# Optimization experiments

Hardware: AMD Instinct MI355X
Metric: run time of the kernel (lower is better)

Reference implementation:

```python
import jax, jax.numpy as jnp
import numpy as np

T, B, H = 256, 64, 1024

def setup_inputs() -> dict:
    key = jax.random.key(0)
    k0, k1, k2, k3 = jax.random.split(key, 4)
    x = jax.random.normal(k0, (T, B, H), dtype=jnp.float32)
    # episode resets are sparse events
    resets = jax.random.bernoulli(k1, 0.01, (T, B))
    h0 = jnp.zeros((B, H), dtype=jnp.float32)  # flax GRUCell.initialize_carry -> zeros
    s = np.float32(1.0 / np.sqrt(H))
    Wi = jax.random.normal(k2, (H, 3 * H), dtype=jnp.float32) * s  # packed [ir|iz|in]
    Wh = jax.random.normal(k3, (H, 3 * H), dtype=jnp.float32) * s  # packed [hr|hz|hn]
    bi = jnp.zeros((3 * H,), dtype=jnp.float32)
    bn = jnp.zeros((H,), dtype=jnp.float32)  # only the 'n' hidden dense has a bias in flax
    return dict(x=x, resets=resets, h0=h0, Wi=Wi, bi=bi, Wh=Wh, bn=bn)

def reference(x, resets, h0, Wi, bi, Wh, bn):
    """Scanned GRU with reset masking, matching flax nn.scan(GRUCell)."""
    def step(h, inp):
        x_t, r_t = inp  # [B,H], [B]
        h = jnp.where(r_t[:, None], jnp.zeros_like(h), h)  # reset carry to initial (zeros)
        gi = x_t @ Wi + bi          # [B,3H]
        gh = h @ Wh                 # [B,3H]
        ir, iz, inn = jnp.split(gi, 3, axis=-1)
        hr, hz, hn = jnp.split(gh, 3, axis=-1)
        r = jax.nn.sigmoid(ir + hr)
        z = jax.nn.sigmoid(iz + hz)
        n = jnp.tanh(inn + r * (hn + bn))
        h_new = (1.0 - z) * n + z * h
        return h_new, h_new  # GRUCell returns (new_state, y=new_state)
    h_final, ys = jax.lax.scan(step, h0, (x, resets))
    return h_final, ys
```

## Files before the change

kernel.cpp:

```cpp
#include <hip/hip_runtime.h>
#include <hip/hip_bf16.h>
#include <cstdint>


#define TT 256
#define BB 64
#define HH 1024
#define H3 3072

typedef __attribute__((ext_vector_type(8))) short s16x8;
typedef __attribute__((ext_vector_type(4))) float f32x4;
typedef __attribute__((ext_vector_type(4))) unsigned int u32x4;
typedef unsigned long long ull;

__device__ __forceinline__ float fast_sigmoid(float x) {
  float e = __expf(-fabsf(x));
  float s = 1.0f / (1.0f + e);
  return x >= 0.0f ? s : 1.0f - s;
}
__device__ __forceinline__ float fast_tanh(float x) {
  float e = __expf(-2.0f * fabsf(x));
  float t = (1.0f - e) / (1.0f + e);
  return x >= 0.0f ? t : -t;
}
__device__ __forceinline__ f32x4 mfma16(s16x8 a, s16x8 b, f32x4 c) {
  return __builtin_amdgcn_mfma_f32_16x16x32_bf16(a, b, c, 0, 0, 0);
}

#define LD8(p) __hip_atomic_load((p), __ATOMIC_RELAXED, __HIP_MEMORY_SCOPE_AGENT)
#define ST8(p, v) __hip_atomic_store((p), (v), __ATOMIC_RELAXED, __HIP_MEMORY_SCOPE_AGENT)

__device__ __forceinline__ u32x4 ld16_opaque(const char* p) {
  u32x4 r;
  asm volatile("global_load_dwordx4 %0, %1, off\n\t"
               "s_waitcnt vmcnt(0)"
               : "=&v"(r) : "v"(p) : "memory");
  return r;
}


__global__ void k_cvt_x(const float* __restrict__ x, __hip_bfloat16* __restrict__ xb, int n) {
  int i = (blockIdx.x * blockDim.x + threadIdx.x) * 4;
  if (i + 3 < n) {
    float4 v = *reinterpret_cast<const float4*>(x + i);
    xb[i + 0] = __float2bfloat16(v.x);
    xb[i + 1] = __float2bfloat16(v.y);
    xb[i + 2] = __float2bfloat16(v.z);
    xb[i + 3] = __float2bfloat16(v.w);
  }
}

__global__ void k_transpose_w(const float* __restrict__ W, __hip_bfloat16* __restrict__ WT) {
  __shared__ float tile[32][33];
  int c0 = blockIdx.x * 32, r0 = blockIdx.y * 32;
  int tx = threadIdx.x & 31, ty = threadIdx.x >> 5;
#pragma unroll
  for (int i = 0; i < 32; i += 8)
    tile[ty + i][tx] = W[(size_t)(r0 + ty + i) * H3 + c0 + tx];
  __syncthreads();
#pragma unroll
  for (int i = 0; i < 32; i += 8)
    WT[(size_t)(c0 + ty + i) * HH + r0 + tx] = __float2bfloat16(tile[tx][ty + i]);
}


template <bool GIF32>
__global__ __launch_bounds__(256, 2) void k_gemm_gi(
    const __hip_bfloat16* __restrict__ A,
    const __hip_bfloat16* __restrict__ Bt,
    const float* __restrict__ bi,
    void* __restrict__ gi)
{
  __shared__ __align__(16) __hip_bfloat16 As[128 * 32];
  __shared__ __align__(16) __hip_bfloat16 Bs[128 * 32];
  const int bid = blockIdx.x;
  const int mt = bid / 24, nt = bid % 24;
  const int m0 = mt * 128, n0 = nt * 128;
  const int tid = threadIdx.x, lane = tid & 63, w = tid >> 6;
  const int wm = w & 1, wn = w >> 1;

  f32x4 acc[4][4];
#pragma unroll
  for (int ai = 0; ai < 4; ++ai)
#pragma unroll
    for (int bj = 0; bj < 4; ++bj) acc[ai][bj] = (f32x4){0.f, 0.f, 0.f, 0.f};

  for (int k0 = 0; k0 < HH; k0 += 32) {
#pragma unroll
    for (int i = 0; i < 2; ++i) {
      const int c = w + i * 4;
      const int idx = c * 64 + lane;
      const int row = idx >> 2, slot = idx & 3;
      __builtin_amdgcn_global_load_lds(
          (const __attribute__((address_space(1))) void*)(A + (size_t)(m0 + row) * HH + k0 + slot * 8),
          (__attribute__((address_space(3))) void*)(As + c * 512), 16, 0, 0);
      __builtin_amdgcn_global_load_lds(
          (const __attribute__((address_space(1))) void*)(Bt + (size_t)(n0 + row) * HH + k0 + slot * 8),
          (__attribute__((address_space(3))) void*)(Bs + c * 512), 16, 0, 0);
    }
    __syncthreads();
    s16x8 af[4], bf[4];
#pragma unroll
    for (int ai = 0; ai < 4; ++ai) {
      int r = wm * 64 + ai * 16 + (lane & 15);
      af[ai] = *reinterpret_cast<const s16x8*>(As + r * 32 + (lane >> 4) * 8);
    }
#pragma unroll
    for (int bj = 0; bj < 4; ++bj) {
      int r = wn * 64 + bj * 16 + (lane & 15);
      bf[bj] = *reinterpret_cast<const s16x8*>(Bs + r * 32 + (lane >> 4) * 8);
    }
#pragma unroll
    for (int ai = 0; ai < 4; ++ai)
#pragma unroll
      for (int bj = 0; bj < 4; ++bj) acc[ai][bj] = mfma16(af[ai], bf[bj], acc[ai][bj]);
    __syncthreads();
  }

#pragma unroll
  for (int ai = 0; ai < 4; ++ai) {
#pragma unroll
    for (int reg = 0; reg < 4; ++reg) {
      const size_t row = (size_t)m0 + wm * 64 + ai * 16 + (lane >> 4) * 4 + reg;
#pragma unroll
      for (int bj = 0; bj < 4; ++bj) {
        const int col = n0 + wn * 64 + bj * 16 + (lane & 15);
        float v = acc[ai][bj][reg] + bi[col];
        if (GIF32)
          reinterpret_cast<float*>(gi)[row * H3 + col] = v;
        else
          reinterpret_cast<__hip_bfloat16*>(gi)[row * H3 + col] = __float2bfloat16(v);
      }
    }
  }
}


template <bool GIF32>
__global__ __launch_bounds__(256, 1) void k_gru(
    const void* __restrict__ gi_,
    const int* __restrict__ resets,
    const float* __restrict__ h0,
    const float* __restrict__ bn,
    const __hip_bfloat16* __restrict__ WhT,
    __hip_bfloat16* hseq,
    float* __restrict__ out)
{
  __shared__ __align__(16) char Wlds[64 * 2048];
  __shared__ __align__(16) f32x4 part[2][4][6][32];
  __shared__ __align__(8) __hip_bfloat16 hsh[8][32];

  const int tid = threadIdx.x;
  const int wave = tid >> 6, lane = tid & 63;
  const int wg = blockIdx.x;
  const int g = wg & 7, s = wg >> 3;
  const int bg0 = g * 8, j0 = s * 32;
  const int l15 = lane & 15;

  const int bl = tid >> 5;
  const int jl = tid & 31;
  const int b = bg0 + bl, j = j0 + jl;
  const float bnj = bn[j];
  float hp = h0[(size_t)b * HH + j];

  hsh[bl][jl] = __float2bfloat16(hp);
  if (lane < 16) {
    const int prow = wave * 2 + (lane >> 3);
    const int pw = lane & 7;
    ull pv = *reinterpret_cast<const ull*>(&hsh[prow][pw * 4]);
    ST8(reinterpret_cast<ull*>(hseq + (size_t)(bg0 + prow) * HH + j0 + pw * 4), pv);
  }

  for (int u = tid; u < 64 * 128; u += 256) {
    const int row = u >> 7, sl = u & 127;
    const int gate = row >> 5, jj = row & 31;
    u32x4 v = *reinterpret_cast<const u32x4*>(WhT + (size_t)(gate * HH + j0 + jj) * HH + sl * 8);
    const int byte = row * 2048 + ((sl * 16) ^ ((row & 7) << 4));
    *reinterpret_cast<u32x4*>(Wlds + byte) = v;
  }

  u32x4 bnf[16];
#pragma unroll
  for (int nt = 0; nt < 2; ++nt)
#pragma unroll
    for (int kk = 0; kk < 8; ++kk)
      bnf[nt * 8 + kk] = ld16_opaque(reinterpret_cast<const char*>(
          WhT + (size_t)(2 * HH + j0 + nt * 16 + l15) * HH + wave * 256 + kk * 32 + (lane >> 4) * 8));

  int rstE = resets[b];
  float giR, giZ, giN;
  if (GIF32) {
    const float* grow = reinterpret_cast<const float*>(gi_) + (size_t)b * H3;
    giR = grow[j]; giZ = grow[HH + j]; giN = grow[2 * HH + j];
  } else {
    const __hip_bfloat16* grow = reinterpret_cast<const __hip_bfloat16*>(gi_) + (size_t)b * H3;
    giR = __bfloat162float(grow[j]);
    giZ = __bfloat162float(grow[HH + j]);
    giN = __bfloat162float(grow[2 * HH + j]);
  }

  const int alr = lane & 7;
  const int koff = (lane >> 4) * 8;
  const int cprod = lane >> 3, crow = lane & 7;
  const size_t cansub = (size_t)(bg0 + crow) * HH + (wave * 8 + cprod) * 32 + 28;

  __syncthreads();

  for (int t = 0; t < TT; ++t) {
    const int p = t & 1;
    const int rstA = resets[t * BB + bg0 + alr];
    const __hip_bfloat16* rd = hseq + (size_t)t * 65536;

    {
      const ull* cp = reinterpret_cast<const ull*>(rd + cansub);
      int gq = 0;
      ull c;
      do {
        c = LD8(cp);
      } while (__any((int)(c == ~0ull)) && ++gq < (1 << 20));
    }

    const ull* ch = reinterpret_cast<const ull*>(
        rd + (size_t)(bg0 + alr) * HH + wave * 256 + koff);
    ull w[16];
#pragma unroll
    for (int kk = 0; kk < 8; ++kk) {
      w[2 * kk + 0] = LD8(ch + kk * 8 + 0);
      w[2 * kk + 1] = LD8(ch + kk * 8 + 1);
    }
    {
      int gq = 0;
      for (;;) {
        unsigned bad = 0;
#pragma unroll
        for (int i = 0; i < 16; ++i) bad |= (unsigned)(w[i] == ~0ull);
        if (!__any((int)bad) || ++gq >= (1 << 18)) break;
#pragma unroll
        for (int kk = 0; kk < 8; ++kk) {
          w[2 * kk + 0] = LD8(ch + kk * 8 + 0);
          w[2 * kk + 1] = LD8(ch + kk * 8 + 1);
        }
      }
    }

    const ull amask = ((l15 < 8) && !rstA) ? ~0ull : 0ull;
    f32x4 acc[6];
#pragma unroll
    for (int tl = 0; tl < 6; ++tl) acc[tl] = (f32x4){0.f, 0.f, 0.f, 0.f};
#pragma unroll
    for (int kk = 0; kk < 8; ++kk) {
      union { ull q[2]; s16x8 v; } u;
      u.q[0] = w[2 * kk + 0] & amask;
      u.q[1] = w[2 * kk + 1] & amask;
      const int kb = wave * 512 + kk * 64 + (lane >> 4) * 16;
#pragma unroll
      for (int nt = 0; nt < 2; ++nt) {
        const int rR = nt * 16 + l15;
        const int rZ = 32 + nt * 16 + l15;
        s16x8 br = *reinterpret_cast<const s16x8*>(Wlds + rR * 2048 + (kb ^ ((rR & 7) << 4)));
        s16x8 bz = *reinterpret_cast<const s16x8*>(Wlds + rZ * 2048 + (kb ^ ((rZ & 7) << 4)));
        acc[0 + nt] = mfma16(u.v, br, acc[0 + nt]);
        acc[2 + nt] = mfma16(u.v, bz, acc[2 + nt]);
        acc[4 + nt] = mfma16(u.v, __builtin_bit_cast(s16x8, bnf[nt * 8 + kk]), acc[4 + nt]);
      }
    }
    if (lane < 32) {
#pragma unroll
      for (int tl = 0; tl < 6; ++tl) part[p][wave][tl][lane] = acc[tl];
    }
    __syncthreads();

    const int nt = jl >> 4;
    const int li = ((bl >> 2) << 4) | (jl & 15), el = bl & 3;
    float sR = part[p][0][0 + nt][li][el];
    float sZ = part[p][0][2 + nt][li][el];
    float sN = part[p][0][4 + nt][li][el];
#pragma unroll
    for (int ww = 1; ww < 4; ++ww) {
      sR += part[p][ww][0 + nt][li][el];
      sZ += part[p][ww][2 + nt][li][el];
      sN += part[p][ww][4 + nt][li][el];
    }
    const float hprev = rstE ? 0.f : hp;
    const float rg = fast_sigmoid(giR + sR);
    const float zg = fast_sigmoid(giZ + sZ);
    const float ng = fast_tanh(giN + rg * (sN + bnj));
    const float hnew = (1.0f - zg) * ng + zg * hprev;
    hp = hnew;

    hsh[bl][jl] = __float2bfloat16(hnew);
    if (lane < 16) {
      const int prow = wave * 2 + (lane >> 3);
      const int pw = lane & 7;
      ull pv = *reinterpret_cast<const ull*>(&hsh[prow][pw * 4]);
      ST8(reinterpret_cast<ull*>(hseq + (size_t)(t + 1) * 65536 +
                                 (size_t)(bg0 + prow) * HH + j0 + pw * 4),
          pv);
    }

    __builtin_nontemporal_store(hnew, out + 65536 + (size_t)t * 65536 + (size_t)b * HH + j);

    const int tn = (t + 1 < TT) ? t + 1 : t;
    rstE = resets[tn * BB + b];
    if (GIF32) {
      const float* grow = reinterpret_cast<const float*>(gi_) + (size_t)(tn * BB + b) * H3;
      giR = grow[j]; giZ = grow[HH + j]; giN = grow[2 * HH + j];
    } else {
      const __hip_bfloat16* grow =
          reinterpret_cast<const __hip_bfloat16*>(gi_) + (size_t)(tn * BB + b) * H3;
      giR = __bfloat162float(grow[j]);
      giZ = __bfloat162float(grow[HH + j]);
      giN = __bfloat162float(grow[2 * HH + j]);
    }
  }

  out[(size_t)b * HH + j] = hp;
}


extern "C" void kernel_launch(void* const* d_in, const int* in_sizes, int n_in,
                              void* d_out, int out_size, void* d_ws, size_t ws_size,
                              hipStream_t stream) {
  const float* x      = (const float*)d_in[0];
  const int* resets   = (const int*)d_in[1];
  const float* h0     = (const float*)d_in[2];
  const float* Wi     = (const float*)d_in[3];
  const float* bi     = (const float*)d_in[4];
  const float* Wh     = (const float*)d_in[5];
  const float* bn     = (const float*)d_in[6];
  (void)in_sizes; (void)n_in; (void)out_size;

  char* ws = (char*)d_ws;
  __hip_bfloat16* xb   = (__hip_bfloat16*)(ws);
  __hip_bfloat16* hseq = (__hip_bfloat16*)(ws);
  __hip_bfloat16* WiT  = (__hip_bfloat16*)(ws + 33685504);
  __hip_bfloat16* WhT  = (__hip_bfloat16*)(ws + 39976960);
  void* gi             = (void*)(ws + 46268416);

  const bool gif32 = ws_size >= 46268416ull + (size_t)16384 * 3072 * 4;

  k_cvt_x<<<16384, 256, 0, stream>>>(x, xb, TT * BB * HH);
  k_transpose_w<<<dim3(96, 32), 256, 0, stream>>>(Wi, WiT);
  k_transpose_w<<<dim3(96, 32), 256, 0, stream>>>(Wh, WhT);
  if (gif32) {
    k_gemm_gi<true><<<3072, 256, 0, stream>>>(xb, WiT, bi, gi);
    hipMemsetAsync(hseq, 0xFF, 33685504, stream);
    k_gru<true><<<256, 256, 0, stream>>>(gi, resets, h0, bn, WhT, hseq, (float*)d_out);
  } else {
    k_gemm_gi<false><<<3072, 256, 0, stream>>>(xb, WiT, bi, gi);
    hipMemsetAsync(hseq, 0xFF, 33685504, stream);
    k_gru<false><<<256, 256, 0, stream>>>(gi, resets, h0, bn, WhT, hseq, (float*)d_out);
  }
}
```

Measured before the change: 1.302 ms.

## Prefetch next-step hidden state speculatively and read own slice from LDS

```diff
diff --git a/kernel.cpp b/kernel.cpp
--- a/kernel.cpp
+++ b/kernel.cpp
@@ -136,6 +136,134 @@
 }
 
 
+#define ISSUE16(W, CH)                                   \
+  do {                                                   \
+    _Pragma("unroll") for (int i_ = 0; i_ < 8; ++i_) {   \
+      W[2 * i_ + 0] = LD8((CH) + i_ * 8 + 0);            \
+      W[2 * i_ + 1] = LD8((CH) + i_ * 8 + 1);            \
+    }                                                    \
+  } while (0)
+
+#define STEP(T, CUR, NXT)                                                      \
+  do {                                                                         \
+    const int t_ = (T);                                                        \
+    const int p_ = t_ & 1;                   \
+    const int ph_ = (t_ + 1) & 1;            \
+    const int rstA_ = resets[t_ * BB + bg0 + alr];                             \
+    const __hip_bfloat16* rd_ = hseq + (size_t)t_ * 65536;                     \
+    {    \
+      const ull* cp_ = reinterpret_cast<const ull*>(rd_ + cansub);             \
+      int gq_ = 0;                                                             \
+      ull c_;                                                                  \
+      do {                                                                     \
+        c_ = LD8(cp_);                                                         \
+      } while (__any((int)(c_ == ~0ull)) && ++gq_ < (1 << 20));                \
+    }                                                                          \
+    {      \
+      unsigned bad_ = 0;                                                       \
+      _Pragma("unroll") for (int i_ = 0; i_ < 16; ++i_)                        \
+        if ((i_ >> 1) != kselfw) bad_ |= (unsigned)(CUR[i_] == ~0ull);         \
+      if (__any((int)bad_)) {                                                  \
+        const ull* ch_ = reinterpret_cast<const ull*>(rd_ + chsub);            \
+        int gq_ = 0;                                                           \
+        for (;;) {                                                             \
+          ISSUE16(CUR, ch_);                                                   \
+          unsigned b2_ = 0;                                                    \
+          _Pragma("unroll") for (int i_ = 0; i_ < 16; ++i_)                    \
+            if ((i_ >> 1) != kselfw) b2_ |= (unsigned)(CUR[i_] == ~0ull);      \
+          if (!__any((int)b2_) || ++gq_ >= (1 << 18)) break;                   \
+        }                                                                      \
+      }                                                                        \
+    }                                                                          \
+     \
+    const ull amask_ = ((l15 < 8) && !rstA_) ? ~0ull : 0ull;                   \
+    f32x4 acc_[6];                                                             \
+    _Pragma("unroll") for (int tl_ = 0; tl_ < 6; ++tl_)                        \
+      acc_[tl_] = (f32x4){0.f, 0.f, 0.f, 0.f};                                 \
+    _Pragma("unroll") for (int kk_ = 0; kk_ < 8; ++kk_) {                      \
+      union { ull q[2]; s16x8 v; } u_;                                         \
+      if (kk_ == kselfw) {                                                     \
+        u_.v = *reinterpret_cast<const s16x8*>(&hsh[ph_][alr][koff]);          \
+        u_.q[0] &= amask_;                                                     \
+        u_.q[1] &= amask_;                                                     \
+      } else {                                                                 \
+        u_.q[0] = CUR[2 * kk_ + 0] & amask_;                                   \
+        u_.q[1] = CUR[2 * kk_ + 1] & amask_;                                   \
+      }                                                                        \
+      const int kb_ = wave * 512 + kk_ * 64 + (lane >> 4) * 16;                \
+      _Pragma("unroll") for (int nt_ = 0; nt_ < 2; ++nt_) {                    \
+        const int rR_ = nt_ * 16 + l15;                                        \
+        const int rZ_ = 32 + nt_ * 16 + l15;                                   \
+        s16x8 br_ = *reinterpret_cast<const s16x8*>(                           \
+            Wlds + rR_ * 2048 + (kb_ ^ ((rR_ & 7) << 4)));                     \
+        s16x8 bz_ = *reinterpret_cast<const s16x8*>(                           \
+            Wlds + rZ_ * 2048 + (kb_ ^ ((rZ_ & 7) << 4)));                     \
+        acc_[0 + nt_] = mfma16(u_.v, br_, acc_[0 + nt_]);                      \
+        acc_[2 + nt_] = mfma16(u_.v, bz_, acc_[2 + nt_]);                      \
+        acc_[4 + nt_] =                                                        \
+            mfma16(u_.v, __builtin_bit_cast(s16x8, bnf[nt_ * 8 + kk_]),        \
+                   acc_[4 + nt_]);                                             \
+      }                                                                        \
+    }                                                                          \
+    if (lane < 32) {                                                           \
+      _Pragma("unroll") for (int tl_ = 0; tl_ < 6; ++tl_)                      \
+        part[p_][wave][tl_][lane] = acc_[tl_];                                 \
+    }                                                                          \
+    __syncthreads();                                                           \
+                         \
+    const int nt_ = jl >> 4;                                                   \
+    const int li_ = ((bl >> 2) << 4) | (jl & 15), el_ = bl & 3;                \
+    float sR_ = part[p_][0][0 + nt_][li_][el_];                                \
+    float sZ_ = part[p_][0][2 + nt_][li_][el_];                                \
+    float sN_ = part[p_][0][4 + nt_][li_][el_];                                \
+    _Pragma("unroll") for (int ww_ = 1; ww_ < 4; ++ww_) {                      \
+      sR_ += part[p_][ww_][0 + nt_][li_][el_];                                 \
+      sZ_ += part[p_][ww_][2 + nt_][li_][el_];                                 \
+      sN_ += part[p_][ww_][4 + nt_][li_][el_];                                 \
+    }                                                                          \
+    const float hprev_ = rstE ? 0.f : hp;                                      \
+    const float rg_ = fast_sigmoid(giR + sR_);                                 \
+    const float zg_ = fast_sigmoid(giZ + sZ_);                                 \
+    const float ng_ = fast_tanh(giN + rg_ * (sN_ + bnj));                      \
+    const float hnew_ = (1.0f - zg_) * ng_ + zg_ * hprev_;                     \
+    hp = hnew_;                                                                \
+    hsh[p_][bl][jl] = __float2bfloat16(hnew_);                                 \
+        \
+    if (lane < 16) {                                                           \
+      const int prow_ = wave * 2 + (lane >> 3);                                \
+      const int pw_ = lane & 7;                                                \
+      ull pv_ = *reinterpret_cast<const ull*>(&hsh[p_][prow_][pw_ * 4]);       \
+      ST8(reinterpret_cast<ull*>(hseq + (size_t)(t_ + 1) * 65536 +             \
+                                 (size_t)(bg0 + prow_) * HH + j0 + pw_ * 4),   \
+          pv_);                                                                \
+    }                                                                          \
+        \
+    {                                                                          \
+      const ull* chn_ = reinterpret_cast<const ull*>(                          \
+          hseq + (size_t)(t_ + 1) * 65536 + chsub);                            \
+      ISSUE16(NXT, chn_);                                                      \
+    }                                                                          \
+                                \
+    __builtin_nontemporal_store(                                               \
+        hnew_, out + 65536 + (size_t)t_ * 65536 + (size_t)b * HH + j);         \
+                                          \
+    const int tn_ = (t_ + 1 < TT) ? t_ + 1 : t_;                               \
+    rstE = resets[tn_ * BB + b];                                               \
+    if (GIF32) {                                                               \
+      const float* grow_ =                                                     \
+          reinterpret_cast<const float*>(gi_) + (size_t)(tn_ * BB + b) * H3;   \
+      giR = grow_[j]; giZ = grow_[HH + j]; giN = grow_[2 * HH + j];            \
+    } else {                                                                   \
+      const __hip_bfloat16* grow_ =                                            \
+          reinterpret_cast<const __hip_bfloat16*>(gi_) +                       \
+          (size_t)(tn_ * BB + b) * H3;                                         \
+      giR = __bfloat162float(grow_[j]);                                        \
+      giZ = __bfloat162float(grow_[HH + j]);                                   \
+      giN = __bfloat162float(grow_[2 * HH + j]);                               \
+    }                                                                          \
+    __syncthreads();        \
+  } while (0)
+
 template <bool GIF32>
 __global__ __launch_bounds__(256, 1) void k_gru(
     const void* __restrict__ gi_,
@@ -148,7 +276,7 @@
 {
   __shared__ __align__(16) char Wlds[64 * 2048];
   __shared__ __align__(16) f32x4 part[2][4][6][32];
-  __shared__ __align__(8) __hip_bfloat16 hsh[8][32];
+  __shared__ __align__(16) __hip_bfloat16 hsh[2][8][32];
 
   const int tid = threadIdx.x;
   const int wave = tid >> 6, lane = tid & 63;
@@ -163,11 +291,11 @@
   const float bnj = bn[j];
   float hp = h0[(size_t)b * HH + j];
 
-  hsh[bl][jl] = __float2bfloat16(hp);
+  hsh[1][bl][jl] = __float2bfloat16(hp);
   if (lane < 16) {
     const int prow = wave * 2 + (lane >> 3);
     const int pw = lane & 7;
-    ull pv = *reinterpret_cast<const ull*>(&hsh[prow][pw * 4]);
+    ull pv = *reinterpret_cast<const ull*>(&hsh[1][prow][pw * 4]);
     ST8(reinterpret_cast<ull*>(hseq + (size_t)(bg0 + prow) * HH + j0 + pw * 4), pv);
   }
 
@@ -201,117 +329,23 @@
 
   const int alr = lane & 7;
   const int koff = (lane >> 4) * 8;
-  const int cprod = lane >> 3, crow = lane & 7;
+  const int kselfw = (wave == (s >> 3)) ? (s & 7) : -1;
+  const int cprod0 = lane >> 3, crow = lane & 7;
+  const int cprod = (cprod0 == kselfw) ? (cprod0 ^ 1) : cprod0;
   const size_t cansub = (size_t)(bg0 + crow) * HH + (wave * 8 + cprod) * 32 + 28;
+  const size_t chsub = (size_t)(bg0 + alr) * HH + wave * 256 + koff;
 
   __syncthreads();
 
-  for (int t = 0; t < TT; ++t) {
-    const int p = t & 1;
-    const int rstA = resets[t * BB + bg0 + alr];
-    const __hip_bfloat16* rd = hseq + (size_t)t * 65536;
-
-    {
-      const ull* cp = reinterpret_cast<const ull*>(rd + cansub);
-      int gq = 0;
-      ull c;
-      do {
-        c = LD8(cp);
-      } while (__any((int)(c == ~0ull)) && ++gq < (1 << 20));
-    }
-
-    const ull* ch = reinterpret_cast<const ull*>(
-        rd + (size_t)(bg0 + alr) * HH + wave * 256 + koff);
-    ull w[16];
-#pragma unroll
-    for (int kk = 0; kk < 8; ++kk) {
-      w[2 * kk + 0] = LD8(ch + kk * 8 + 0);
-      w[2 * kk + 1] = LD8(ch + kk * 8 + 1);
-    }
-    {
-      int gq = 0;
-      for (;;) {
-        unsigned bad = 0;
-#pragma unroll
-        for (int i = 0; i < 16; ++i) bad |= (unsigned)(w[i] == ~0ull);
-        if (!__any((int)bad) || ++gq >= (1 << 18)) break;
-#pragma unroll
-        for (int kk = 0; kk < 8; ++kk) {
-          w[2 * kk + 0] = LD8(ch + kk * 8 + 0);
-          w[2 * kk + 1] = LD8(ch + kk * 8 + 1);
-        }
-      }
-    }
-
-    const ull amask = ((l15 < 8) && !rstA) ? ~0ull : 0ull;
-    f32x4 acc[6];
-#pragma unroll
-    for (int tl = 0; tl < 6; ++tl) acc[tl] = (f32x4){0.f, 0.f, 0.f, 0.f};
-#pragma unroll
-    for (int kk = 0; kk < 8; ++kk) {
-      union { ull q[2]; s16x8 v; } u;
-      u.q[0] = w[2 * kk + 0] & amask;
-      u.q[1] = w[2 * kk + 1] & amask;
-      const int kb = wave * 512 + kk * 64 + (lane >> 4) * 16;
-#pragma unroll
-      for (int nt = 0; nt < 2; ++nt) {
-        const int rR = nt * 16 + l15;
-        const int rZ = 32 + nt * 16 + l15;
-        s16x8 br = *reinterpret_cast<const s16x8*>(Wlds + rR * 2048 + (kb ^ ((rR & 7) << 4)));
-        s16x8 bz = *reinterpret_cast<const s16x8*>(Wlds + rZ * 2048 + (kb ^ ((rZ & 7) << 4)));
-        acc[0 + nt] = mfma16(u.v, br, acc[0 + nt]);
-        acc[2 + nt] = mfma16(u.v, bz, acc[2 + nt]);
-        acc[4 + nt] = mfma16(u.v, __builtin_bit_cast(s16x8, bnf[nt * 8 + kk]), acc[4 + nt]);
-      }
-    }
-    if (lane < 32) {
-#pragma unroll
-      for (int tl = 0; tl < 6; ++tl) part[p][wave][tl][lane] = acc[tl];
-    }
-    __syncthreads();
-
-    const int nt = jl >> 4;
-    const int li = ((bl >> 2) << 4) | (jl & 15), el = bl & 3;
-    float sR = part[p][0][0 + nt][li][el];
-    float sZ = part[p][0][2 + nt][li][el];
-    float sN = part[p][0][4 + nt][li][el];
-#pragma unroll
-    for (int ww = 1; ww < 4; ++ww) {
-      sR += part[p][ww][0 + nt][li][el];
-      sZ += part[p][ww][2 + nt][li][el];
-      sN += part[p][ww][4 + nt][li][el];
-    }
-    const float hprev = rstE ? 0.f : hp;
-    const float rg = fast_sigmoid(giR + sR);
-    const float zg = fast_sigmoid(giZ + sZ);
-    const float ng = fast_tanh(giN + rg * (sN + bnj));
-    const float hnew = (1.0f - zg) * ng + zg * hprev;
-    hp = hnew;
-
-    hsh[bl][jl] = __float2bfloat16(hnew);
-    if (lane < 16) {
-      const int prow = wave * 2 + (lane >> 3);
-      const int pw = lane & 7;
-      ull pv = *reinterpret_cast<const ull*>(&hsh[prow][pw * 4]);
-      ST8(reinterpret_cast<ull*>(hseq + (size_t)(t + 1) * 65536 +
-                                 (size_t)(bg0 + prow) * HH + j0 + pw * 4),
-          pv);
-    }
-
-    __builtin_nontemporal_store(hnew, out + 65536 + (size_t)t * 65536 + (size_t)b * HH + j);
-
-    const int tn = (t + 1 < TT) ? t + 1 : t;
-    rstE = resets[tn * BB + b];
-    if (GIF32) {
-      const float* grow = reinterpret_cast<const float*>(gi_) + (size_t)(tn * BB + b) * H3;
-      giR = grow[j]; giZ = grow[HH + j]; giN = grow[2 * HH + j];
-    } else {
-      const __hip_bfloat16* grow =
-          reinterpret_cast<const __hip_bfloat16*>(gi_) + (size_t)(tn * BB + b) * H3;
-      giR = __bfloat162float(grow[j]);
-      giZ = __bfloat162float(grow[HH + j]);
-      giN = __bfloat162float(grow[2 * HH + j]);
-    }
+  ull wA[16], wB[16];
+  {
+    const ull* ch0 = reinterpret_cast<const ull*>(hseq + chsub);
+    ISSUE16(wA, ch0);
+  }
+
+  for (int t = 0; t < TT; t += 2) {
+    STEP(t, wA, wB);
+    STEP(t + 1, wB, wA);
   }
 
   out[(size_t)b * HH + j] = hp;
```

New measurement: 1.661 ms. 1.28x slower.
